# Kernel tuning notes

Hardware: AMD Instinct MI355X
Metric: run time of the kernel (lower is better)

Reference implementation:

```python
import jax, jax.numpy as jnp
import numpy as np
from jax import lax

B, C, O, H, W = 4, 96, 96, 128, 128
K = 3      # kernel size everywhere
D = 2      # dilation of dconv
KK = K * K


def conv2d(x, w, b, pad, dil=1):
    # x: [B,C,H,W], w: [O,C,K,K]
    y = lax.conv_general_dilated(
        x, w, window_strides=(1, 1), padding=[(pad, pad), (pad, pad)],
        rhs_dilation=(dil, dil), dimension_numbers=('NCHW', 'OIHW', 'NCHW'))
    return y + b[None, :, None, None]


def bilinear_sample(img, py, px):
    # img: [B,C,H,W]; py,px: [B,KK,H,W] float sample coords (zero outside)
    y0 = jnp.floor(py)
    x0 = jnp.floor(px)
    wy = py - y0
    wx = px - x0
    flat = img.reshape(B, 1, C, H * W)  # broadcast over KK

    def gather(yi, xi):
        valid = (yi >= 0) & (yi < H) & (xi >= 0) & (xi < W)
        yc = jnp.clip(yi, 0, H - 1).astype(jnp.int32)
        xc = jnp.clip(xi, 0, W - 1).astype(jnp.int32)
        idx = (yc * W + xc).reshape(B, KK, 1, H * W)
        g = jnp.take_along_axis(flat, idx, axis=3)  # [B,KK,C,H*W]
        g = g.reshape(B, KK, C, H, W)
        return g * valid.reshape(B, KK, 1, H, W)

    v00 = gather(y0, x0)
    v01 = gather(y0, x0 + 1)
    v10 = gather(y0 + 1, x0)
    v11 = gather(y0 + 1, x0 + 1)
    wy = wy[:, :, None]
    wx = wx[:, :, None]
    return ((1 - wy) * ((1 - wx) * v00 + wx * v01)
            + wy * ((1 - wx) * v10 + wx * v11))


def setup_inputs() -> dict:
    key = jax.random.key(0)
    ks = jax.random.split(key, 7)
    x = jax.random.normal(ks[0], (B, C, H, W), jnp.float32)
    s = 1.0 / np.sqrt(C * K * K)  # torch default conv init bound
    u = lambda k, shape: jax.random.uniform(k, shape, jnp.float32, -s, s)
    return dict(
        x=x,
        dconv_w=u(ks[1], (O, C, K, K)), dconv_b=u(ks[2], (O,)),
        off_w=u(ks[3], (2 * KK, C, K, K)), off_b=u(ks[4], (2 * KK,)),
        def_w=u(ks[5], (O, C, K, K)), def_b=u(ks[6], (O,)),
    )


def reference(x, dconv_w, dconv_b, off_w, off_b, def_w, def_b):
    # dilated conv + relu + residual (self.conv is unused in the original forward)
    x1 = conv2d(x, dconv_w, dconv_b, pad=D, dil=D)
    x3 = x + jax.nn.relu(x1)

    # offset prediction: [B, 2*KK, H, W] -> (dy, dx) per kernel tap
    offset = conv2d(x3, off_w, off_b, pad=1)
    off = offset.reshape(B, KK, 2, H, W)
    dy, dx = off[:, :, 0], off[:, :, 1]

    # base sampling grid: output pixel + kernel tap - padding
    ki, kj = jnp.meshgrid(jnp.arange(K), jnp.arange(K), indexing='ij')
    ky = (ki.reshape(-1) - (K - 1) // 2).astype(jnp.float32)  # [KK]
    kx = (kj.reshape(-1) - (K - 1) // 2).astype(jnp.float32)
    ygrid = jnp.arange(H, dtype=jnp.float32)[:, None]
    xgrid = jnp.arange(W, dtype=jnp.float32)[None, :]
    py = ygrid[None, None] + ky[None, :, None, None] + dy  # [B,KK,H,W]
    px = xgrid[None, None] + kx[None, :, None, None] + dx

    sampled = bilinear_sample(x3, py, px)  # [B,KK,C,H,W]
    out = jnp.einsum('bkchw,ock->bohw', sampled, def_w.reshape(O, C, KK))
    return out + def_b[None, :, None, None]
```

## Files before the change

kernel.cpp:

```cpp
#include <hip/hip_runtime.h>
#include <hip/hip_bf16.h>

#define BD 4
#define CD 96
#define OD 96
#define HD 128
#define WD 128
#define HWD (HD*WD)

typedef __attribute__((ext_vector_type(8))) short bfrag;
typedef __attribute__((ext_vector_type(4))) float ffrag;

__device__ __forceinline__ short f2bs(float f) {
    __hip_bfloat16 h = __float2bfloat16(f);
    return *reinterpret_cast<short*>(&h);
}

__device__ __forceinline__ bfrag interp4(bfrag c00, bfrag c01, bfrag c10, bfrag c11,
                                         float f00, float f01, float f10, float f11) {
    const int* i00 = (const int*)&c00;
    const int* i01 = (const int*)&c01;
    const int* i10 = (const int*)&c10;
    const int* i11 = (const int*)&c11;
    int ap[4];
    #pragma unroll
    for (int d = 0; d < 4; d++) {
        float a0 = __int_as_float(((unsigned)i00[d]) << 16);
        float b0 = __int_as_float(((unsigned)i01[d]) << 16);
        float c0 = __int_as_float(((unsigned)i10[d]) << 16);
        float d0 = __int_as_float(((unsigned)i11[d]) << 16);
        float a1 = __int_as_float(i00[d] & 0xffff0000);
        float b1 = __int_as_float(i01[d] & 0xffff0000);
        float c1 = __int_as_float(i10[d] & 0xffff0000);
        float d1 = __int_as_float(i11[d] & 0xffff0000);
        float rlo = f00*a0 + f01*b0 + f10*c0 + f11*d0;
        float rhi = f00*a1 + f01*b1 + f10*c1 + f11*d1;
        ap[d] = (int)((unsigned short)f2bs(rlo)) |
                ((int)((unsigned short)f2bs(rhi)) << 16);
    }
    return *(const bfrag*)ap;
}

__device__ __forceinline__ int swizzle512(int gid) {
    return ((gid & 7) << 6) | (gid >> 3);
}

__global__ __launch_bounds__(256) void k_transpose(const float* __restrict__ x,
                                                   short* __restrict__ xb16) {
    __shared__ short tile[64 * 104];
    int pix0 = blockIdx.x * 64;
    int b = pix0 / HWD; int hw0 = pix0 % HWD;
    int tid = threadIdx.x;

    for (int e = tid; e < 96*16; e += 256) {
        int c = e >> 4, g = e & 15;
        float4 v = *(const float4*)(x + ((size_t)(b*96 + c))*HWD + hw0 + 4*g);
        tile[(4*g+0)*104 + c] = f2bs(v.x);
        tile[(4*g+1)*104 + c] = f2bs(v.y);
        tile[(4*g+2)*104 + c] = f2bs(v.z);
        tile[(4*g+3)*104 + c] = f2bs(v.w);
    }
    __syncthreads();
    for (int e = tid; e < 64*12; e += 256) {
        int px = e / 12, c8 = e % 12;
        bfrag v = *(const bfrag*)(tile + px*104 + c8*8);
        *(bfrag*)(xb16 + ((size_t)(pix0 + px))*96 + c8*8) = v;
    }
}

__global__ void k_repack(const float* __restrict__ dconv_w,
                         const float* __restrict__ off_w,
                         const float* __restrict__ def_w,
                         short* __restrict__ wB1,
                         short* __restrict__ wB2,
                         short* __restrict__ wB) {
    int t = blockIdx.x * blockDim.x + threadIdx.x;
    if (t < 27648) {
        int j = t & 7; int l = (t >> 3) & 63; int tile = t >> 9;
        int s = tile >> 1, nt = tile & 1;
        int k = 32*s + (l >> 4)*8 + j;
        int o = 16*nt + (l & 15);
        int c = k % 96, tap = k / 96;
        wB2[t] = (o < 18) ? f2bs(off_w[(o*96 + c)*9 + tap]) : (short)0;
    }
    if (t < 82944) {
        int j = t & 7; int l = (t >> 3) & 63; int tile = t >> 9;
        int s = tile / 6, nt = tile % 6;
        int k = 32*s + (l >> 4)*8 + j;
        int o = 16*nt + (l & 15);
        int c = k % 96, tap = k / 96;
        wB1[t] = f2bs(dconv_w[(o*96 + c)*9 + tap]);
        wB[t]  = f2bs(def_w [(o*96 + c)*9 + tap]);
    }
}

#define SLICE_SHORTS 9216

__global__ __launch_bounds__(512, 2) void k_conv1(const float* __restrict__ x,
                                                  const short* __restrict__ xb16,
                                                  const short* __restrict__ wB,
                                                  const float* __restrict__ bias,
                                                  short* __restrict__ x3b) {
    __shared__ short wbuf[2][SLICE_SHORTS];

    int pix0 = swizzle512(blockIdx.x) * 128;
    int b = pix0 / HWD; int hw0 = pix0 % HWD;
    int h = hw0 / WD;
    int tid = threadIdx.x;
    int l = tid & 63, wv = tid >> 6;
    int q = l >> 4, mr = l & 15;
    int px0w = 16*wv;
    const char* xbc = (const char*)(xb16 + ((size_t)b * HWD) * 96);
    const bfrag az = {0,0,0,0,0,0,0,0};

    {
        bfrag s0, s1, s2;
        int c2 = tid + 1024;
        s0 = *(const bfrag*)(wB + tid*8);
        s1 = *(const bfrag*)(wB + (tid+512)*8);
        if (c2 < 1152) s2 = *(const bfrag*)(wB + c2*8);
        *(bfrag*)&wbuf[0][tid*8]       = s0;
        *(bfrag*)&wbuf[0][(tid+512)*8] = s1;
        if (c2 < 1152) *(bfrag*)&wbuf[0][c2*8] = s2;
    }
    __syncthreads();

    ffrag acc[6];
    #pragma unroll
    for (int nt = 0; nt < 6; nt++) acc[nt] = ffrag{0.f,0.f,0.f,0.f};

    int cur = 0;
    #pragma unroll 1
    for (int tap = 0; tap < 9; tap++) {
        bfrag s0, s1, s2;
        if (tap < 8) {
            const short* src = wB + (size_t)(tap+1)*SLICE_SHORTS;
            int c2 = tid + 1024;
            s0 = *(const bfrag*)(src + tid*8);
            s1 = *(const bfrag*)(src + (tid+512)*8);
            if (c2 < 1152) s2 = *(const bfrag*)(src + c2*8);
        }

        int y = h + (tap/3)*2 - 2;
        int yc = min(max(y, 0), HD-1);
        int xx = px0w + mr + (tap%3)*2 - 2;
        int xxc = min(max(xx, 0), WD-1);
        bool v = ((unsigned)y < HD) && ((unsigned)xx < WD);
        unsigned aoff = (unsigned)(((yc*WD + xxc)*96 + q*8) * 2);
        #pragma unroll
        for (int sc = 0; sc < 3; sc++) {
            bfrag a = *(const bfrag*)(xbc + aoff + sc*64);
            if (!v) a = az;
            const short* wp = &wbuf[cur][(sc*6)*512 + l*8];
            #pragma unroll
            for (int nt = 0; nt < 6; nt++) {
                bfrag bb = *(const bfrag*)(wp + nt*512);
                acc[nt] = __builtin_amdgcn_mfma_f32_16x16x32_bf16(a, bb, acc[nt], 0, 0, 0);
            }
        }

        if (tap < 8) {
            int c2 = tid + 1024;
            *(bfrag*)&wbuf[cur^1][tid*8]       = s0;
            *(bfrag*)&wbuf[cur^1][(tid+512)*8] = s1;
            if (c2 < 1152) *(bfrag*)&wbuf[cur^1][c2*8] = s2;
        }
        __syncthreads();
        cur ^= 1;
    }

    short (*etile)[104] = (short(*)[104])&wbuf[0][0];
    {
        int lrow = px0w + q*4;
        int hwb = hw0 + lrow;
        #pragma unroll
        for (int nt = 0; nt < 6; nt++) {
            int o = 16*nt + mr;
            float bo = bias[o];
            float4 xr = *(const float4*)(x + ((size_t)(b*96 + o))*HWD + hwb);
            etile[lrow+0][o] = f2bs(xr.x + fmaxf(acc[nt][0] + bo, 0.f));
            etile[lrow+1][o] = f2bs(xr.y + fmaxf(acc[nt][1] + bo, 0.f));
            etile[lrow+2][o] = f2bs(xr.z + fmaxf(acc[nt][2] + bo, 0.f));
            etile[lrow+3][o] = f2bs(xr.w + fmaxf(acc[nt][3] + bo, 0.f));
        }
    }
    __syncthreads();
    for (int e = tid; e < 128*12; e += 512) {
        int px = e / 12, c8 = e % 12;
        bfrag v = *(const bfrag*)&etile[px][c8*8];
        *(bfrag*)(x3b + ((size_t)(b*HWD + hw0 + px))*96 + c8*8) = v;
    }
}

__global__ __launch_bounds__(512, 2) void k_deform(const short* __restrict__ x3b,
                                                   const short* __restrict__ wB2,
                                                   const float* __restrict__ off_b,
                                                   const short* __restrict__ wB,
                                                   const float* __restrict__ def_b,
                                                   float* __restrict__ out) {
    __shared__ __align__(16) char smem[36864 + 12288];
    short (*wbuf)[SLICE_SHORTS] = (short(*)[SLICE_SHORTS])smem;
    short* cb = (short*)(smem + 36864);
    float (*offsb)[20] = (float(*)[20])(smem + 36864);

    int pix0 = swizzle512(blockIdx.x) * 128;
    int b = pix0 / HWD; int hw0 = pix0 % HWD;
    int h = hw0 / WD;
    int tid = threadIdx.x;
    int l = tid & 63, wv = tid >> 6;
    int q = l >> 4, mr = l & 15;
    int px0w = 16*wv;
    const char* xbc = (const char*)(x3b + ((size_t)b * HWD) * 96);
    const bfrag az = {0,0,0,0,0,0,0,0};

    {
        bfrag s0, s1, s2;
        int c2 = tid + 1024;
        s0 = *(const bfrag*)(wB + tid*8);
        s1 = *(const bfrag*)(wB + (tid+512)*8);
        if (c2 < 1152) s2 = *(const bfrag*)(wB + c2*8);
        *(bfrag*)&wbuf[0][tid*8]       = s0;
        *(bfrag*)&wbuf[0][(tid+512)*8] = s1;
        if (c2 < 1152) *(bfrag*)&wbuf[0][c2*8] = s2;
        if (tid < 384) {
            bfrag sc2 = *(const bfrag*)(wB2 + tid*8);
            *(bfrag*)&cb[tid*8] = sc2;
        }
    }
    __syncthreads();

    ffrag oa0 = ffrag{0.f,0.f,0.f,0.f};
    ffrag oa1 = ffrag{0.f,0.f,0.f,0.f};

    int c2cur = 0;
    #pragma unroll 1
    for (int tap = 0; tap < 9; tap++) {
        bfrag sn;
        bool act = (tid < 384) && (tap < 8);
        if (act) sn = *(const bfrag*)(wB2 + (size_t)(tap+1)*3072 + tid*8);

        int y = h + tap/3 - 1;
        int yc = min(max(y, 0), HD-1);
        int xx = px0w + mr + tap%3 - 1;
        int xxc = min(max(xx, 0), WD-1);
        bool v = ((unsigned)y < HD) && ((unsigned)xx < WD);
        unsigned aoff = (unsigned)(((yc*WD + xxc)*96 + q*8) * 2);
        #pragma unroll
        for (int sc = 0; sc < 3; sc++) {
            const short* wb = cb + c2cur*3072 + (sc*2)*512 + l*8;
            bfrag b0 = *(const bfrag*)(wb);
            bfrag b1 = *(const bfrag*)(wb + 512);
            bfrag a = *(const bfrag*)(xbc + aoff + sc*64);
            if (!v) a = az;
            oa0 = __builtin_amdgcn_mfma_f32_16x16x32_bf16(a, b0, oa0, 0, 0, 0);
            oa1 = __builtin_amdgcn_mfma_f32_16x16x32_bf16(a, b1, oa1, 0, 0, 0);
        }

        if (act) *(bfrag*)&cb[(c2cur^1)*3072 + tid*8] = sn;
        __syncthreads();
        c2cur ^= 1;
    }

    {
        int row = px0w + q*4;
        float bo0 = off_b[mr];
        #pragma unroll
        for (int r = 0; r < 4; r++) offsb[row + r][mr] = oa0[r] + bo0;
        if (mr < 2) {
            float bo1 = off_b[16 + mr];
            #pragma unroll
            for (int r = 0; r < 4; r++) offsb[row + r][16 + mr] = oa1[r] + bo1;
        }
    }

    ffrag acc[6];
    #pragma unroll
    for (int nt = 0; nt < 6; nt++) acc[nt] = ffrag{0.f,0.f,0.f,0.f};

    int cur = 0;
    #pragma unroll 1
    for (int tap = 0; tap < 9; tap++) {
        bfrag s0, s1, s2;
        if (tap < 8) {
            const short* src = wB + (size_t)(tap+1)*SLICE_SHORTS;
            int c2 = tid + 1024;
            s0 = *(const bfrag*)(src + tid*8);
            s1 = *(const bfrag*)(src + (tid+512)*8);
            if (c2 < 1152) s2 = *(const bfrag*)(src + c2*8);
        }

        unsigned po[4];
        float fbv[4];
        {
            int lp = px0w + mr;
            float dy = offsb[lp][2*tap];
            float dx = offsb[lp][2*tap + 1];
            float py  = (float)(h  + tap/3 - 1) + dy;
            float pxf = (float)(lp + tap%3 - 1) + dx;
            float y0f = floorf(py), x0f = floorf(pxf);
            float wy = py - y0f, wx = pxf - x0f;
            int y0 = (int)y0f, x0 = (int)x0f;
            int y1 = y0 + 1, x1 = x0 + 1;
            bool vy0 = (unsigned)y0 < HD, vy1 = (unsigned)y1 < HD;
            bool vx0 = (unsigned)x0 < WD, vx1 = (unsigned)x1 < WD;
            fbv[0] = (vy0 && vx0) ? (1.f-wy)*(1.f-wx) : 0.f;
            fbv[1] = (vy0 && vx1) ? (1.f-wy)*wx       : 0.f;
            fbv[2] = (vy1 && vx0) ? wy*(1.f-wx)       : 0.f;
            fbv[3] = (vy1 && vx1) ? wy*wx             : 0.f;
            int yc0 = min(max(y0,0),HD-1), yc1 = min(max(y1,0),HD-1);
            int xc0 = min(max(x0,0),WD-1), xc1 = min(max(x1,0),WD-1);
            po[0] = (unsigned)(((yc0*WD + xc0)*96 + q*8)*2);
            po[1] = (unsigned)(((yc0*WD + xc1)*96 + q*8)*2);
            po[2] = (unsigned)(((yc1*WD + xc0)*96 + q*8)*2);
            po[3] = (unsigned)(((yc1*WD + xc1)*96 + q*8)*2);
        }
        #pragma unroll
        for (int sc = 0; sc < 3; sc++) {
            const short* wp = &wbuf[cur][(sc*6)*512 + l*8];
            bfrag bbf[6];
            #pragma unroll
            for (int nt = 0; nt < 6; nt++) bbf[nt] = *(const bfrag*)(wp + nt*512);
            bfrag c00 = *(const bfrag*)(xbc + po[0] + sc*64);
            bfrag c01 = *(const bfrag*)(xbc + po[1] + sc*64);
            bfrag c10 = *(const bfrag*)(xbc + po[2] + sc*64);
            bfrag c11 = *(const bfrag*)(xbc + po[3] + sc*64);
            bfrag a = interp4(c00, c01, c10, c11, fbv[0], fbv[1], fbv[2], fbv[3]);
            #pragma unroll
            for (int nt = 0; nt < 6; nt++)
                acc[nt] = __builtin_amdgcn_mfma_f32_16x16x32_bf16(a, bbf[nt], acc[nt], 0, 0, 0);
        }

        if (tap < 8) {
            int c2 = tid + 1024;
            *(bfrag*)&wbuf[cur^1][tid*8]       = s0;
            *(bfrag*)&wbuf[cur^1][(tid+512)*8] = s1;
            if (c2 < 1152) *(bfrag*)&wbuf[cur^1][c2*8] = s2;
        }
        __syncthreads();
        cur ^= 1;
    }

    int hwb = hw0 + px0w + q*4;
    #pragma unroll
    for (int nt = 0; nt < 6; nt++) {
        int o = 16*nt + mr;
        float bo = def_b[o];
        float4 v;
        v.x = acc[nt][0] + bo; v.y = acc[nt][1] + bo;
        v.z = acc[nt][2] + bo; v.w = acc[nt][3] + bo;
        *(float4*)(out + ((size_t)(b*96 + o))*HWD + hwb) = v;
    }
}

extern "C" void kernel_launch(void* const* d_in, const int* in_sizes, int n_in,
                              void* d_out, int out_size, void* d_ws, size_t ws_size,
                              hipStream_t stream) {
    const float* x       = (const float*)d_in[0];
    const float* dconv_w = (const float*)d_in[1];
    const float* dconv_b = (const float*)d_in[2];
    const float* off_w   = (const float*)d_in[3];
    const float* off_b   = (const float*)d_in[4];
    const float* def_w   = (const float*)d_in[5];
    const float* def_b   = (const float*)d_in[6];
    float* out = (float*)d_out;

    char* ws = (char*)d_ws;
    short* xb16 = (short*)(ws);
    short* x3b  = (short*)(ws + 12582912);
    short* wB1  = (short*)(ws + 25165824);
    short* wB2  = (short*)(ws + 25331712);
    short* wB   = (short*)(ws + 25387008);

    k_repack<<<324, 256, 0, stream>>>(dconv_w, off_w, def_w, wB1, wB2, wB);
    k_transpose<<<(BD*HWD)/64, 256, 0, stream>>>(x, xb16);
    k_conv1<<<(BD*HWD)/128, 512, 0, stream>>>(x, xb16, wB1, dconv_b, x3b);
    k_deform<<<(BD*HWD)/128, 512, 0, stream>>>(x3b, wB2, off_b, wB, def_b, out);
}
```

Baseline: 160.7 us.

## Split bf16 NHWC activations into three 32-channel planes for aligned 64-byte gathers

```diff
diff --git a/kernel.cpp b/kernel.cpp
--- a/kernel.cpp
+++ b/kernel.cpp
@@ -7,6 +7,7 @@
 #define HD 128
 #define WD 128
 #define HWD (HD*WD)
+#define PLANEB ((size_t)(BD*HWD)*64)
 
 typedef __attribute__((ext_vector_type(8))) short bfrag;
 typedef __attribute__((ext_vector_type(4))) float ffrag;
@@ -46,7 +47,7 @@
 }
 
 __global__ __launch_bounds__(256) void k_transpose(const float* __restrict__ x,
-                                                   short* __restrict__ xb16) {
+                                                   char* __restrict__ xbP) {
     __shared__ short tile[64 * 104];
     int pix0 = blockIdx.x * 64;
     int b = pix0 / HWD; int hw0 = pix0 % HWD;
@@ -63,8 +64,9 @@
     __syncthreads();
     for (int e = tid; e < 64*12; e += 256) {
         int px = e / 12, c8 = e % 12;
+        int sc = c8 >> 2, ck = c8 & 3;
         bfrag v = *(const bfrag*)(tile + px*104 + c8*8);
-        *(bfrag*)(xb16 + ((size_t)(pix0 + px))*96 + c8*8) = v;
+        *(bfrag*)(xbP + (size_t)sc*PLANEB + ((size_t)(pix0 + px))*64 + ck*16) = v;
     }
 }
 
@@ -97,10 +99,10 @@
 #define SLICE_SHORTS 9216
 
 __global__ __launch_bounds__(512, 2) void k_conv1(const float* __restrict__ x,
-                                                  const short* __restrict__ xb16,
+                                                  const char* __restrict__ xbP,
                                                   const short* __restrict__ wB,
                                                   const float* __restrict__ bias,
-                                                  short* __restrict__ x3b) {
+                                                  char* __restrict__ x3P) {
     __shared__ short wbuf[2][SLICE_SHORTS];
 
     int pix0 = swizzle512(blockIdx.x) * 128;
@@ -110,7 +112,6 @@
     int l = tid & 63, wv = tid >> 6;
     int q = l >> 4, mr = l & 15;
     int px0w = 16*wv;
-    const char* xbc = (const char*)(xb16 + ((size_t)b * HWD) * 96);
     const bfrag az = {0,0,0,0,0,0,0,0};
 
     {
@@ -146,10 +147,10 @@
         int xx = px0w + mr + (tap%3)*2 - 2;
         int xxc = min(max(xx, 0), WD-1);
         bool v = ((unsigned)y < HD) && ((unsigned)xx < WD);
-        unsigned aoff = (unsigned)(((yc*WD + xxc)*96 + q*8) * 2);
+        size_t u = ((size_t)(b*HWD + yc*WD + xxc))*64 + q*16;
         #pragma unroll
         for (int sc = 0; sc < 3; sc++) {
-            bfrag a = *(const bfrag*)(xbc + aoff + sc*64);
+            bfrag a = *(const bfrag*)(xbP + (size_t)sc*PLANEB + u);
             if (!v) a = az;
             const short* wp = &wbuf[cur][(sc*6)*512 + l*8];
             #pragma unroll
@@ -187,12 +188,13 @@
     __syncthreads();
     for (int e = tid; e < 128*12; e += 512) {
         int px = e / 12, c8 = e % 12;
+        int sc = c8 >> 2, ck = c8 & 3;
         bfrag v = *(const bfrag*)&etile[px][c8*8];
-        *(bfrag*)(x3b + ((size_t)(b*HWD + hw0 + px))*96 + c8*8) = v;
-    }
-}
-
-__global__ __launch_bounds__(512, 2) void k_deform(const short* __restrict__ x3b,
+        *(bfrag*)(x3P + (size_t)sc*PLANEB + ((size_t)(b*HWD + hw0 + px))*64 + ck*16) = v;
+    }
+}
+
+__global__ __launch_bounds__(512, 2) void k_deform(const char* __restrict__ x3P,
                                                    const short* __restrict__ wB2,
                                                    const float* __restrict__ off_b,
                                                    const short* __restrict__ wB,
@@ -210,7 +212,6 @@
     int l = tid & 63, wv = tid >> 6;
     int q = l >> 4, mr = l & 15;
     int px0w = 16*wv;
-    const char* xbc = (const char*)(x3b + ((size_t)b * HWD) * 96);
     const bfrag az = {0,0,0,0,0,0,0,0};
 
     {
@@ -244,13 +245,13 @@
         int xx = px0w + mr + tap%3 - 1;
         int xxc = min(max(xx, 0), WD-1);
         bool v = ((unsigned)y < HD) && ((unsigned)xx < WD);
-        unsigned aoff = (unsigned)(((yc*WD + xxc)*96 + q*8) * 2);
+        size_t u = ((size_t)(b*HWD + yc*WD + xxc))*64 + q*16;
         #pragma unroll
         for (int sc = 0; sc < 3; sc++) {
             const short* wb = cb + c2cur*3072 + (sc*2)*512 + l*8;
             bfrag b0 = *(const bfrag*)(wb);
             bfrag b1 = *(const bfrag*)(wb + 512);
-            bfrag a = *(const bfrag*)(xbc + aoff + sc*64);
+            bfrag a = *(const bfrag*)(x3P + (size_t)sc*PLANEB + u);
             if (!v) a = az;
             oa0 = __builtin_amdgcn_mfma_f32_16x16x32_bf16(a, b0, oa0, 0, 0, 0);
             oa1 = __builtin_amdgcn_mfma_f32_16x16x32_bf16(a, b1, oa1, 0, 0, 0);
@@ -289,7 +290,7 @@
             if (c2 < 1152) s2 = *(const bfrag*)(src + c2*8);
         }
 
-        unsigned po[4];
+        size_t po[4];
         float fbv[4];
         {
             int lp = px0w + mr;
@@ -309,21 +310,22 @@
             fbv[3] = (vy1 && vx1) ? wy*wx             : 0.f;
             int yc0 = min(max(y0,0),HD-1), yc1 = min(max(y1,0),HD-1);
             int xc0 = min(max(x0,0),WD-1), xc1 = min(max(x1,0),WD-1);
-            po[0] = (unsigned)(((yc0*WD + xc0)*96 + q*8)*2);
-            po[1] = (unsigned)(((yc0*WD + xc1)*96 + q*8)*2);
-            po[2] = (unsigned)(((yc1*WD + xc0)*96 + q*8)*2);
-            po[3] = (unsigned)(((yc1*WD + xc1)*96 + q*8)*2);
+            po[0] = ((size_t)(b*HWD + yc0*WD + xc0))*64 + q*16;
+            po[1] = ((size_t)(b*HWD + yc0*WD + xc1))*64 + q*16;
+            po[2] = ((size_t)(b*HWD + yc1*WD + xc0))*64 + q*16;
+            po[3] = ((size_t)(b*HWD + yc1*WD + xc1))*64 + q*16;
         }
         #pragma unroll
         for (int sc = 0; sc < 3; sc++) {
+            const char* pb = x3P + (size_t)sc*PLANEB;
             const short* wp = &wbuf[cur][(sc*6)*512 + l*8];
             bfrag bbf[6];
             #pragma unroll
             for (int nt = 0; nt < 6; nt++) bbf[nt] = *(const bfrag*)(wp + nt*512);
-            bfrag c00 = *(const bfrag*)(xbc + po[0] + sc*64);
-            bfrag c01 = *(const bfrag*)(xbc + po[1] + sc*64);
-            bfrag c10 = *(const bfrag*)(xbc + po[2] + sc*64);
-            bfrag c11 = *(const bfrag*)(xbc + po[3] + sc*64);
+            bfrag c00 = *(const bfrag*)(pb + po[0]);
+            bfrag c01 = *(const bfrag*)(pb + po[1]);
+            bfrag c10 = *(const bfrag*)(pb + po[2]);
+            bfrag c11 = *(const bfrag*)(pb + po[3]);
             bfrag a = interp4(c00, c01, c10, c11, fbv[0], fbv[1], fbv[2], fbv[3]);
             #pragma unroll
             for (int nt = 0; nt < 6; nt++)
@@ -365,14 +367,14 @@
     float* out = (float*)d_out;
 
     char* ws = (char*)d_ws;
-    short* xb16 = (short*)(ws);
-    short* x3b  = (short*)(ws + 12582912);
+    char*  xbP  = ws;
+    char*  x3P  = ws + 12582912;
     short* wB1  = (short*)(ws + 25165824);
     short* wB2  = (short*)(ws + 25331712);
     short* wB   = (short*)(ws + 25387008);
 
     k_repack<<<324, 256, 0, stream>>>(dconv_w, off_w, def_w, wB1, wB2, wB);
-    k_transpose<<<(BD*HWD)/64, 256, 0, stream>>>(x, xb16);
-    k_conv1<<<(BD*HWD)/128, 512, 0, stream>>>(x, xb16, wB1, dconv_b, x3b);
-    k_deform<<<(BD*HWD)/128, 512, 0, stream>>>(x3b, wB2, off_b, wB, def_b, out);
-}
+    k_transpose<<<(BD*HWD)/64, 256, 0, stream>>>(x, xbP);
+    k_conv1<<<(BD*HWD)/128, 512, 0, stream>>>(x, xbP, wB1, dconv_b, x3P);
+    k_deform<<<(BD*HWD)/128, 512, 0, stream>>>(x3P, wB2, off_b, wB, def_b, out);
+}
```

After: 156.6 us, median of 2. -2.5%, faster.
